# Optimization experiments

Hardware: AMD Instinct MI355X
Metric: run time of the kernel (lower is better)

## Reference

```python
import jax, jax.numpy as jnp
import numpy as np

NUM_GRAPHS = 512
N_NODES = 100000
N_EDGES = 1600000
D_NODE = 128
D_EDGE = 32
D_OUT = 64


def setup_inputs() -> dict:
    key = jax.random.key(0)
    k = jax.random.split(key, 6)
    x = jax.random.normal(k[0], (N_NODES, D_NODE), dtype=jnp.float32)
    edge_index = jax.random.randint(k[1], (2, N_EDGES), 0, N_NODES, dtype=jnp.int64)
    edge_attr = jax.random.normal(k[2], (N_EDGES, D_EDGE), dtype=jnp.float32)
    u = jax.random.normal(k[3], (NUM_GRAPHS, D_OUT), dtype=jnp.float32)
    batch = jnp.sort(jax.random.randint(k[4], (N_NODES,), 0, NUM_GRAPHS, dtype=jnp.int64))
    W = jax.random.normal(k[5], (D_NODE + D_EDGE, D_OUT), dtype=jnp.float32) * 0.05
    b = jnp.full((D_OUT,), 0.01, dtype=jnp.float32)
    return {"x": x, "edge_index": edge_index, "edge_attr": edge_attr, "u": u, "batch": batch, "W": W, "b": b}


def reference(x, edge_index, edge_attr, u, batch, W, b):
    # row, col = edge_index; only col is used
    col = edge_index[1]
    # scatter_add nodes by graph id -> [B, D_NODE]
    node_aggregate = jax.ops.segment_sum(x, batch, num_segments=NUM_GRAPHS)
    # scatter_add edges by graph id of target node -> [B, D_EDGE]
    edge_aggregate = jax.ops.segment_sum(edge_attr, batch[col], num_segments=NUM_GRAPHS)
    out = jnp.concatenate([node_aggregate, edge_aggregate], axis=1)  # [B, 160]
    return out @ W + b  # [B, 64]
```

## Files before the change

### kernel.cpp

```cpp
#include <hip/hip_runtime.h>

#define NUM_GRAPHS 512
#define N_NODES 100000
#define N_EDGES 1600000
#define D_NODE 128
#define D_EDGE 32
#define D_OUT 64

#define NBLK 512
#define EPB (N_EDGES / NBLK)
#define SLOTS 32
#define GCAP 5120

__global__ __launch_bounds__(512) void count_place_kernel(const int* __restrict__ col,
                                                          const int* __restrict__ batch,
                                                          int* __restrict__ cnt,
                                                          int* __restrict__ bucket) {
    __shared__ int cur[NUM_GRAPHS];
    const int t = threadIdx.x, b = blockIdx.x;
    cur[t] = 0;
    __syncthreads();
    const int base = b * EPB;
    #pragma unroll
    for (int r = 0; r < 7; ++r) {
        const int i = r * 512 + t;
        if (i < EPB) {
            const int e = base + i;
            const int g = batch[col[e]];
            const int s = atomicAdd(&cur[g], 1);
            if (s < SLOTS) bucket[(((size_t)b << 9) + g) * SLOTS + s] = e;
        }
    }
    __syncthreads();
    cnt[b * NUM_GRAPHS + t] = cur[t];
}

__global__ __launch_bounds__(1024) void fused_kernel(const float* __restrict__ x,
                                                     const int* __restrict__ batch,
                                                     const float* __restrict__ edge_attr,
                                                     const int* __restrict__ cnt,
                                                     const int* __restrict__ bucket,
                                                     const float* __restrict__ W,
                                                     const float* __restrict__ bias,
                                                     float* __restrict__ out) {
    const int g = blockIdx.x;
    const int t = threadIdx.x;
    __shared__ int ids[GCAP];
    __shared__ float4 red[1024];
    __shared__ float4 red2[64];
    __shared__ __align__(16) float feat[D_NODE + D_EDGE];
    __shared__ int wtot[8], wbase[8], ntot_s;

    int n = 0;
    if (t < NBLK) n = cnt[t * NUM_GRAPHS + g];
    n = min(n, SLOTS);

    int l = 0, r = N_NODES;
    while (l < r) { int m = (l + r) >> 1; if (batch[m] < g) l = m + 1; else r = m; }
    const int lo = l;
    r = N_NODES;
    while (l < r) { int m = (l + r) >> 1; if (batch[m] < g + 1) l = m + 1; else r = m; }
    const int hi = l;

    const float4* x4 = reinterpret_cast<const float4*>(x);
    const int d4 = t & 31, rr = t >> 5;
    float4 a = make_float4(0.f, 0.f, 0.f, 0.f);
    for (int i = lo + rr; i < hi; i += 32) {
        const float4 v = x4[(size_t)i * 32 + d4];
        a.x += v.x; a.y += v.y; a.z += v.z; a.w += v.w;
    }
    red[t] = a;

    const int lane = t & 63, w = t >> 6;
    int v = n;
    #pragma unroll
    for (int off = 1; off < 64; off <<= 1) {
        const int u = __shfl_up(v, off, 64);
        if (lane >= off) v += u;
    }
    if (t < NBLK && lane == 63) wtot[w] = v;
    __syncthreads();
    if (t == 0) {
        int s = 0;
        #pragma unroll
        for (int i2 = 0; i2 < 8; ++i2) { wbase[i2] = s; s += wtot[i2]; }
        ntot_s = (s > GCAP) ? GCAP : s;
    }
    if (t < 32) {
        float4 s = red[t];
        #pragma unroll
        for (int p = 1; p < 32; ++p) {
            const float4 u = red[p * 32 + t];
            s.x += u.x; s.y += u.y; s.z += u.z; s.w += u.w;
        }
        reinterpret_cast<float4*>(feat)[t] = s;
    }
    __syncthreads();

    if (t < NBLK && n > 0) {
        int p = wbase[w] + (v - n);
        const int* src = bucket + (((size_t)t << 9) + g) * SLOTS;
        for (int j = 0; j < n; ++j) {
            const int q = p + j;
            if (q < GCAP) ids[q] = src[j];
        }
    }
    __syncthreads();
    const int ntot = ntot_s;

    const float4* ea4 = reinterpret_cast<const float4*>(edge_attr);
    const int slot0 = t >> 3, dq = t & 7;
    float4 a0 = make_float4(0.f, 0.f, 0.f, 0.f);
    float4 a1 = make_float4(0.f, 0.f, 0.f, 0.f);
    float4 a2 = make_float4(0.f, 0.f, 0.f, 0.f);
    float4 a3 = make_float4(0.f, 0.f, 0.f, 0.f);
    for (int base = 0; base < ntot; base += 512) {
        const int s0 = base + slot0, s1 = s0 + 128, s2 = s0 + 256, s3 = s0 + 384;
        const int id0 = (s0 < ntot) ? ids[s0] : -1;
        const int id1 = (s1 < ntot) ? ids[s1] : -1;
        const int id2 = (s2 < ntot) ? ids[s2] : -1;
        const int id3 = (s3 < ntot) ? ids[s3] : -1;
        if (id0 >= 0) { const float4 u = ea4[(size_t)id0 * 8 + dq]; a0.x += u.x; a0.y += u.y; a0.z += u.z; a0.w += u.w; }
        if (id1 >= 0) { const float4 u = ea4[(size_t)id1 * 8 + dq]; a1.x += u.x; a1.y += u.y; a1.z += u.z; a1.w += u.w; }
        if (id2 >= 0) { const float4 u = ea4[(size_t)id2 * 8 + dq]; a2.x += u.x; a2.y += u.y; a2.z += u.z; a2.w += u.w; }
        if (id3 >= 0) { const float4 u = ea4[(size_t)id3 * 8 + dq]; a3.x += u.x; a3.y += u.y; a3.z += u.z; a3.w += u.w; }
    }
    a0.x += a1.x + a2.x + a3.x;
    a0.y += a1.y + a2.y + a3.y;
    a0.z += a1.z + a2.z + a3.z;
    a0.w += a1.w + a2.w + a3.w;
    __syncthreads();
    red[t] = a0;
    __syncthreads();
    if (t < 64) {
        const int part = t >> 3, dq2 = t & 7;
        float4 s = make_float4(0.f, 0.f, 0.f, 0.f);
        #pragma unroll
        for (int k = 0; k < 16; ++k) {
            const float4 u = red[(part * 16 + k) * 8 + dq2];
            s.x += u.x; s.y += u.y; s.z += u.z; s.w += u.w;
        }
        red2[t] = s;
    }
    __syncthreads();
    if (t < 8) {
        float4 s = red2[t];
        #pragma unroll
        for (int k = 1; k < 8; ++k) {
            const float4 u = red2[k * 8 + t];
            s.x += u.x; s.y += u.y; s.z += u.z; s.w += u.w;
        }
        reinterpret_cast<float4*>(feat + D_NODE)[t] = s;
    }
    __syncthreads();

    if (t < D_OUT) {
        float o = bias[t];
        #pragma unroll 8
        for (int k = 0; k < D_NODE + D_EDGE; ++k)
            o += feat[k] * W[k * D_OUT + t];
        out[g * D_OUT + t] = o;
    }
}

extern "C" void kernel_launch(void* const* d_in, const int* in_sizes, int n_in,
                              void* d_out, int out_size, void* d_ws, size_t ws_size,
                              hipStream_t stream) {
    const float* x          = (const float*)d_in[0];
    const int*   edge_index = (const int*)d_in[1];
    const float* edge_attr  = (const float*)d_in[2];
    const int*   batch      = (const int*)d_in[4];
    const float* W          = (const float*)d_in[5];
    const float* b          = (const float*)d_in[6];
    float* out = (float*)d_out;

    const int* col = edge_index + N_EDGES;

    int* cnt    = (int*)d_ws;
    int* bucket = cnt + NBLK * NUM_GRAPHS;

    count_place_kernel<<<NBLK, 512, 0, stream>>>(col, batch, cnt, bucket);
    fused_kernel<<<NUM_GRAPHS, 1024, 0, stream>>>(x, batch, edge_attr, cnt, bucket, W, b, out);
}
```

Baseline: 97.93 us.

## Replace fixed-slot per-block buckets with count-scan-place compact bucketing

```diff
diff --git a/kernel.cpp b/kernel.cpp
--- a/kernel.cpp
+++ b/kernel.cpp
@@ -9,51 +9,100 @@
 
 #define NBLK 512
 #define EPB (N_EDGES / NBLK)
-#define SLOTS 32
 #define GCAP 5120
 
-__global__ __launch_bounds__(512) void count_place_kernel(const int* __restrict__ col,
-                                                          const int* __restrict__ batch,
-                                                          int* __restrict__ cnt,
-                                                          int* __restrict__ bucket) {
+__global__ __launch_bounds__(512) void count_kernel(const int* __restrict__ col,
+                                                    const int* __restrict__ batch,
+                                                    int* __restrict__ eg,
+                                                    int* __restrict__ cntT) {
     __shared__ int cur[NUM_GRAPHS];
     const int t = threadIdx.x, b = blockIdx.x;
     cur[t] = 0;
     __syncthreads();
     const int base = b * EPB;
-    #pragma unroll
-    for (int r = 0; r < 7; ++r) {
+
+    int c[6], gg[6];
+    #pragma unroll
+    for (int r = 0; r < 6; ++r) c[r] = col[base + r * 512 + t];
+    #pragma unroll
+    for (int r = 0; r < 6; ++r) gg[r] = batch[c[r]];
+    #pragma unroll
+    for (int r = 0; r < 6; ++r) {
+        eg[base + r * 512 + t] = gg[r];
+        atomicAdd(&cur[gg[r]], 1);
+    }
+    if (t < EPB - 3072) {
+        const int g = batch[col[base + 3072 + t]];
+        eg[base + 3072 + t] = g;
+        atomicAdd(&cur[g], 1);
+    }
+    __syncthreads();
+    cntT[t * NBLK + b] = cur[t];
+}
+
+__global__ __launch_bounds__(512) void scan_kernel(const int* __restrict__ cntT,
+                                                   int* __restrict__ pos,
+                                                   int* __restrict__ totals) {
+    const int g = blockIdx.x, t = threadIdx.x;
+    const int n = cntT[g * NBLK + t];
+    const int lane = t & 63, w = t >> 6;
+    __shared__ int wtot[8], wbase[8];
+    int v = n;
+    #pragma unroll
+    for (int off = 1; off < 64; off <<= 1) {
+        const int u = __shfl_up(v, off, 64);
+        if (lane >= off) v += u;
+    }
+    if (lane == 63) wtot[w] = v;
+    __syncthreads();
+    if (t == 0) {
+        int s = 0;
+        #pragma unroll
+        for (int i = 0; i < 8; ++i) { wbase[i] = s; s += wtot[i]; }
+    }
+    __syncthreads();
+    pos[t * NUM_GRAPHS + g] = g * GCAP + wbase[w] + v - n;
+    if (t == 511) totals[g] = wbase[7] + v;
+}
+
+__global__ __launch_bounds__(512) void place_kernel(const int* __restrict__ eg,
+                                                    const int* __restrict__ pos,
+                                                    int* __restrict__ bucket) {
+    __shared__ int cur[NUM_GRAPHS];
+    const int t = threadIdx.x, b = blockIdx.x;
+    cur[t] = pos[b * NUM_GRAPHS + t];
+    __syncthreads();
+    const int base = b * EPB;
+    #pragma unroll
+    for (int r = 0; r < 6; ++r) {
         const int i = r * 512 + t;
-        if (i < EPB) {
-            const int e = base + i;
-            const int g = batch[col[e]];
-            const int s = atomicAdd(&cur[g], 1);
-            if (s < SLOTS) bucket[(((size_t)b << 9) + g) * SLOTS + s] = e;
-        }
-    }
-    __syncthreads();
-    cnt[b * NUM_GRAPHS + t] = cur[t];
+        const int g = eg[base + i];
+        const int s = atomicAdd(&cur[g], 1);
+        bucket[s] = base + i;
+    }
+    if (t < EPB - 3072) {
+        const int i = 3072 + t;
+        const int g = eg[base + i];
+        bucket[atomicAdd(&cur[g], 1)] = base + i;
+    }
 }
 
 __global__ __launch_bounds__(1024) void fused_kernel(const float* __restrict__ x,
                                                      const int* __restrict__ batch,
                                                      const float* __restrict__ edge_attr,
-                                                     const int* __restrict__ cnt,
+                                                     const int* __restrict__ totals,
                                                      const int* __restrict__ bucket,
                                                      const float* __restrict__ W,
                                                      const float* __restrict__ bias,
                                                      float* __restrict__ out) {
     const int g = blockIdx.x;
     const int t = threadIdx.x;
-    __shared__ int ids[GCAP];
     __shared__ float4 red[1024];
     __shared__ float4 red2[64];
     __shared__ __align__(16) float feat[D_NODE + D_EDGE];
-    __shared__ int wtot[8], wbase[8], ntot_s;
-
-    int n = 0;
-    if (t < NBLK) n = cnt[t * NUM_GRAPHS + g];
-    n = min(n, SLOTS);
+
+    const int ntot = min(totals[g], GCAP);
+    const int* brow = bucket + g * GCAP;
 
     int l = 0, r = N_NODES;
     while (l < r) { int m = (l + r) >> 1; if (batch[m] < g) l = m + 1; else r = m; }
@@ -70,22 +119,7 @@
         a.x += v.x; a.y += v.y; a.z += v.z; a.w += v.w;
     }
     red[t] = a;
-
-    const int lane = t & 63, w = t >> 6;
-    int v = n;
-    #pragma unroll
-    for (int off = 1; off < 64; off <<= 1) {
-        const int u = __shfl_up(v, off, 64);
-        if (lane >= off) v += u;
-    }
-    if (t < NBLK && lane == 63) wtot[w] = v;
-    __syncthreads();
-    if (t == 0) {
-        int s = 0;
-        #pragma unroll
-        for (int i2 = 0; i2 < 8; ++i2) { wbase[i2] = s; s += wtot[i2]; }
-        ntot_s = (s > GCAP) ? GCAP : s;
-    }
+    __syncthreads();
     if (t < 32) {
         float4 s = red[t];
         #pragma unroll
@@ -96,17 +130,6 @@
         reinterpret_cast<float4*>(feat)[t] = s;
     }
     __syncthreads();
-
-    if (t < NBLK && n > 0) {
-        int p = wbase[w] + (v - n);
-        const int* src = bucket + (((size_t)t << 9) + g) * SLOTS;
-        for (int j = 0; j < n; ++j) {
-            const int q = p + j;
-            if (q < GCAP) ids[q] = src[j];
-        }
-    }
-    __syncthreads();
-    const int ntot = ntot_s;
 
     const float4* ea4 = reinterpret_cast<const float4*>(edge_attr);
     const int slot0 = t >> 3, dq = t & 7;
@@ -116,10 +139,10 @@
     float4 a3 = make_float4(0.f, 0.f, 0.f, 0.f);
     for (int base = 0; base < ntot; base += 512) {
         const int s0 = base + slot0, s1 = s0 + 128, s2 = s0 + 256, s3 = s0 + 384;
-        const int id0 = (s0 < ntot) ? ids[s0] : -1;
-        const int id1 = (s1 < ntot) ? ids[s1] : -1;
-        const int id2 = (s2 < ntot) ? ids[s2] : -1;
-        const int id3 = (s3 < ntot) ? ids[s3] : -1;
+        const int id0 = (s0 < ntot) ? brow[s0] : -1;
+        const int id1 = (s1 < ntot) ? brow[s1] : -1;
+        const int id2 = (s2 < ntot) ? brow[s2] : -1;
+        const int id3 = (s3 < ntot) ? brow[s3] : -1;
         if (id0 >= 0) { const float4 u = ea4[(size_t)id0 * 8 + dq]; a0.x += u.x; a0.y += u.y; a0.z += u.z; a0.w += u.w; }
         if (id1 >= 0) { const float4 u = ea4[(size_t)id1 * 8 + dq]; a1.x += u.x; a1.y += u.y; a1.z += u.z; a1.w += u.w; }
         if (id2 >= 0) { const float4 u = ea4[(size_t)id2 * 8 + dq]; a2.x += u.x; a2.y += u.y; a2.z += u.z; a2.w += u.w; }
@@ -129,7 +152,6 @@
     a0.y += a1.y + a2.y + a3.y;
     a0.z += a1.z + a2.z + a3.z;
     a0.w += a1.w + a2.w + a3.w;
-    __syncthreads();
     red[t] = a0;
     __syncthreads();
     if (t < 64) {
@@ -176,9 +198,14 @@
 
     const int* col = edge_index + N_EDGES;
 
-    int* cnt    = (int*)d_ws;
-    int* bucket = cnt + NBLK * NUM_GRAPHS;
-
-    count_place_kernel<<<NBLK, 512, 0, stream>>>(col, batch, cnt, bucket);
-    fused_kernel<<<NUM_GRAPHS, 1024, 0, stream>>>(x, batch, edge_attr, cnt, bucket, W, b, out);
-}
+    int* eg     = (int*)d_ws;
+    int* cntT   = eg + N_EDGES;
+    int* pos    = cntT + NUM_GRAPHS * NBLK;
+    int* totals = pos + NBLK * NUM_GRAPHS;
+    int* bucket = totals + NUM_GRAPHS;
+
+    count_kernel<<<NBLK, 512, 0, stream>>>(col, batch, eg, cntT);
+    scan_kernel<<<NUM_GRAPHS, 512, 0, stream>>>(cntT, pos, totals);
+    place_kernel<<<NBLK, 512, 0, stream>>>(eg, pos, bucket);
+    fused_kernel<<<NUM_GRAPHS, 1024, 0, stream>>>(x, batch, edge_attr, totals, bucket, W, b, out);
+}
```

Result: faster. 83.71 us (-14.5%).
